# Performance work log

Hardware: AMD Instinct MI355X
Metric: run time of the kernel (lower is better)

## Reference

```python
import jax, jax.numpy as jnp
import numpy as np
from jax import lax

INPUT_SIZE = 256
HIDDEN_SIZE = 512
NUM_LAYERS = 2
T = 2048
B = 64


def setup_inputs() -> dict:
    key = jax.random.key(0)
    k1, k2, k3, k4, k5 = jax.random.split(key, 5)
    fan_g = INPUT_SIZE + HIDDEN_SIZE
    inp = {
        "input": jax.random.normal(k1, (T, B, INPUT_SIZE), dtype=jnp.float32),
        "gate_w": jax.random.uniform(k2, (HIDDEN_SIZE, fan_g), dtype=jnp.float32,
                                     minval=-1.0, maxval=1.0) / np.sqrt(fan_g),
        "gate_b": jax.random.uniform(k3, (HIDDEN_SIZE,), dtype=jnp.float32,
                                     minval=-1.0, maxval=1.0) / np.sqrt(fan_g),
        "out_w": jax.random.uniform(k4, (INPUT_SIZE, HIDDEN_SIZE), dtype=jnp.float32,
                                    minval=-1.0, maxval=1.0) / np.sqrt(HIDDEN_SIZE),
        "out_b": jax.random.uniform(k5, (INPUT_SIZE,), dtype=jnp.float32,
                                    minval=-1.0, maxval=1.0) / np.sqrt(HIDDEN_SIZE),
        "name": 0,  # unused forward arg in the original module
    }
    return inp


def reference(input, gate_w, gate_b, out_w, out_b, name):
    # input: [T, B, input_size]
    batch = input.shape[1]
    h0 = jnp.zeros((batch, HIDDEN_SIZE), dtype=jnp.float32)
    c0 = jnp.zeros((batch, HIDDEN_SIZE), dtype=jnp.float32)

    def step(carry, x_t):
        h, c = carry
        combined = jnp.concatenate([h, x_t], axis=1)          # [B, H+I]
        g = combined @ gate_w.T + gate_b
        s = jax.nn.sigmoid(g)                                 # f = i = o = sigmoid(g)
        ch = jnp.tanh(g)                                      # cell_helper
        c = c * s + ch * s
        h = jnp.tanh(c) * s
        return (h, c), None

    carry = (h0, c0)
    # hidden/cell carry over across layers; every layer re-consumes the same input
    for _ in range(NUM_LAYERS):
        carry, _ = lax.scan(step, carry, input)
    h, _ = carry
    output = h @ out_w.T + out_b                              # [B, input_size]
    return output
```

## Files before the change

### kernel.cpp

```cpp
#include <hip/hip_runtime.h>
#include <stdint.h>

#define T_STEPS 2048
#define BATCH   64
#define IN_SZ   256
#define HID     512
#define FANG    768
#define NLAYER  2
#define TOT_STEPS (T_STEPS*NLAYER)

typedef _Float16 h2 __attribute__((ext_vector_type(2)));
typedef unsigned long long u64;
typedef unsigned int u32;

__device__ __forceinline__ float dot2f(h2 a, h2 b, float c) {
#if __has_builtin(__builtin_amdgcn_fdot2)
    return __builtin_amdgcn_fdot2(a, b, c, false);
#else
    return c + (float)a.x * (float)b.x + (float)a.y * (float)b.y;
#endif
}

__device__ __forceinline__ u32 packh2(float a, float b) {
    h2 t{(_Float16)a, (_Float16)b};
    return __builtin_bit_cast(u32, t);
}
__device__ __forceinline__ h2 bch2(float v) { return __builtin_bit_cast(h2, v); }
__device__ __forceinline__ h2 bch2u(u32 v)  { return __builtin_bit_cast(h2, v); }

__device__ __forceinline__ u64 ld_llc(const u64* p) {
    return __hip_atomic_load(p, __ATOMIC_RELAXED, __HIP_MEMORY_SCOPE_AGENT);
}
__device__ __forceinline__ void st_llc(u64* p, u64 v) {
    __hip_atomic_store(p, v, __ATOMIC_RELAXED, __HIP_MEMORY_SCOPE_AGENT);
}

template<int CTRL>
__device__ __forceinline__ float dpp_add(float x) {
    int xi = __builtin_bit_cast(int, x);
    int yi = __builtin_amdgcn_update_dpp(0, xi, CTRL, 0xf, 0xf, true);
    return x + __builtin_bit_cast(float, yi);
}
__device__ __forceinline__ float reduce4(float x) {
    x = dpp_add<0xB1>(x);
    x = dpp_add<0x4E>(x);
    return x;
}

__global__ __launch_bounds__(256) void xproj_kernel(
    const float* __restrict__ input,
    const float* __restrict__ gate_w,
    const float* __restrict__ gate_b,
    u32* __restrict__ xp16)
{
    __shared__ _Float16 Bs[64][264];
    __shared__ _Float16 As[64][264];

    const int jt = blockIdx.x;
    const int mg = blockIdx.y;
    const int tid = threadIdx.x;
    const int tx = tid & 15, ty = tid >> 4;
    const int j0 = jt * 64;

    #pragma unroll
    for (int l = 0; l < 16; ++l) {
        int e = tid + l * 256;
        int i = e >> 6, kq = e & 63;
        float4 v = *(const float4*)&gate_w[(size_t)(j0 + i) * FANG + HID + kq * 4];
        *(h2*)&Bs[i][kq * 4]     = h2{(_Float16)v.x, (_Float16)v.y};
        *(h2*)&Bs[i][kq * 4 + 2] = h2{(_Float16)v.z, (_Float16)v.w};
    }

    const float4 gb = *(const float4*)&gate_b[j0 + tx * 4];

    for (int mt = 0; mt < 32; ++mt) {
        const int m0 = (mg * 32 + mt) * 64;
        __syncthreads();
        #pragma unroll
        for (int l = 0; l < 16; ++l) {
            int e = tid + l * 256;
            int i = e >> 6, kq = e & 63;
            float4 v = *(const float4*)&input[(size_t)(m0 + i) * IN_SZ + kq * 4];
            *(h2*)&As[i][kq * 4]     = h2{(_Float16)v.x, (_Float16)v.y};
            *(h2*)&As[i][kq * 4 + 2] = h2{(_Float16)v.z, (_Float16)v.w};
        }
        __syncthreads();

        float acc[4][4] = {};
        #pragma unroll
        for (int q = 0; q < 32; ++q) {
            const int k = ((q + tx) & 31) * 8;
            float4 av[4], bv[4];
            #pragma unroll
            for (int i = 0; i < 4; ++i)  av[i] = *(const float4*)&As[ty * 4 + i][k];
            #pragma unroll
            for (int jj = 0; jj < 4; ++jj) bv[jj] = *(const float4*)&Bs[tx * 4 + jj][k];
            #pragma unroll
            for (int i = 0; i < 4; ++i) {
                h2 a0 = bch2(av[i].x), a1 = bch2(av[i].y);
                h2 a2 = bch2(av[i].z), a3 = bch2(av[i].w);
                #pragma unroll
                for (int jj = 0; jj < 4; ++jj) {
                    acc[i][jj] = dot2f(a0, bch2(bv[jj].x), acc[i][jj]);
                    acc[i][jj] = dot2f(a1, bch2(bv[jj].y), acc[i][jj]);
                    acc[i][jj] = dot2f(a2, bch2(bv[jj].z), acc[i][jj]);
                    acc[i][jj] = dot2f(a3, bch2(bv[jj].w), acc[i][jj]);
                }
            }
        }

        #pragma unroll
        for (int i = 0; i < 4; ++i) {
            uint2 ww = { packh2(acc[i][0] + gb.x, acc[i][1] + gb.y),
                         packh2(acc[i][2] + gb.z, acc[i][3] + gb.w) };
            *(uint2*)&xp16[(size_t)(m0 + ty * 4 + i) * 256 + ((j0 + tx * 4) >> 1)] = ww;
        }
    }
}

__global__ __launch_bounds__(512, 2) void lstm_kernel(
    const float* __restrict__ gate_w,
    const u32* __restrict__ xp16,
    u64* __restrict__ hx)
{
    const int blk = blockIdx.x;
    const int s   = blk >> 6;
    const int b   = blk & 63;
    const int tid = threadIdx.x;
    const int r   = tid >> 2;
    const int c   = tid & 3;
    const int j   = s * 128 + r;

    __shared__ u32 hl[2][264];

    h2 w2[64];
    #pragma unroll
    for (int u = 0; u < 16; ++u) {
        const int q = (s * 4 + u) & 15;
        const float* wr = gate_w + (size_t)j * FANG + (q * 16 + c * 4) * 2;
        float4 v0 = *(const float4*)(wr);
        float4 v1 = *(const float4*)(wr + 4);
        w2[u * 4 + 0] = h2{(_Float16)v0.x, (_Float16)v0.y};
        w2[u * 4 + 1] = h2{(_Float16)v0.z, (_Float16)v0.w};
        w2[u * 4 + 2] = h2{(_Float16)v1.x, (_Float16)v1.y};
        w2[u * 4 + 3] = h2{(_Float16)v1.z, (_Float16)v1.w};
    }

    const int si  = tid >> 6;
    const int qs  = si + (si >= s);
    const int prw = qs * 64 + (tid & 63);

    if (tid < 264) hl[0][tid] = 0;

    float cval = 0.0f;

    for (int st = 0; st < TOT_STEPS; ++st) {
        const int t   = st & (T_STEPS - 1);
        const int buf = st & 1;

        u32 xw = 0;
        if (c == 0) xw = xp16[((size_t)t * BATCH + b) * 256 + s * 64 + (r >> 1)];

        const u64* pp = hx + ((size_t)buf * BATCH + b) * 256 + prw;
        u64 pv = 0;
        if (tid < 192) pv = ld_llc(pp);

        __syncthreads();

        float p0 = 0.f, p1 = 0.f, p2 = 0.f, p3 = 0.f;
        #pragma unroll
        for (int u = 0; u < 4; ++u) {
            const int q = s * 4 + u;
            float4 rv = *(const float4*)&hl[buf][q * 16 + c * 4];
            p0 = dot2f(w2[u * 4 + 0], bch2(rv.x), p0);
            p1 = dot2f(w2[u * 4 + 1], bch2(rv.y), p1);
            p2 = dot2f(w2[u * 4 + 2], bch2(rv.z), p2);
            p3 = dot2f(w2[u * 4 + 3], bch2(rv.w), p3);
        }

        if (tid < 192) {
            u64 v = pv;
            int spin = 0;
            while ((u32)(v >> 32) != (u32)st) {
                v = ld_llc(pp);
                if (++spin > (1 << 16)) break;
                if (spin > 64) __builtin_amdgcn_s_sleep(1);
            }
            hl[buf][prw] = (u32)v;
        }
        __syncthreads();

        #pragma unroll
        for (int u = 4; u < 16; ++u) {
            const int q = (s * 4 + u) & 15;
            float4 rv = *(const float4*)&hl[buf][q * 16 + c * 4];
            p0 = dot2f(w2[u * 4 + 0], bch2(rv.x), p0);
            p1 = dot2f(w2[u * 4 + 1], bch2(rv.y), p1);
            p2 = dot2f(w2[u * 4 + 2], bch2(rv.z), p2);
            p3 = dot2f(w2[u * 4 + 3], bch2(rv.w), p3);
        }
        float p = (p0 + p1) + (p2 + p3);
        p = reduce4(p);

        float hf = 0.0f;
        if (c == 0) {
            h2 xp = bch2u(xw);
            float gg = p + (float)((r & 1) ? xp.y : xp.x);
            gg = fminf(fmaxf(gg, -30.0f), 30.0f);
            float sg = 1.0f / (1.0f + __expf(-gg));
            float e2 = __expf(2.0f * gg);
            float ch = (e2 - 1.0f) / (e2 + 1.0f);
            cval = cval * sg + ch * sg;
            float ca = fminf(fmaxf(cval, -15.0f), 15.0f);
            float e3 = __expf(2.0f * ca);
            hf = ((e3 - 1.0f) / (e3 + 1.0f)) * sg;
        }
        float hfo = __shfl_down(hf, 4);
        if ((tid & 7) == 0) {
            const int w = s * 64 + (r >> 1);
            u32 pk = packh2(hf, hfo);
            st_llc(hx + ((size_t)((st + 1) & 1) * BATCH + b) * 256 + w,
                   (u64)pk | ((u64)(u32)(st + 1) << 32));
            hl[buf ^ 1][w] = pk;
        }
    }
}

__global__ __launch_bounds__(256) void out_kernel(
    const u64* __restrict__ hx,
    const float* __restrict__ out_w,
    const float* __restrict__ out_b,
    float* __restrict__ out)
{
    const int b  = blockIdx.x;
    const int jt = threadIdx.x;
    __shared__ float hrow[512];

    {
        u64 v = hx[(size_t)b * 256 + jt];
        h2 pr = bch2u((u32)v);
        hrow[2 * jt]     = (float)pr.x;
        hrow[2 * jt + 1] = (float)pr.y;
    }
    __syncthreads();

    float acc = out_b[jt];
    const float* wr = out_w + (size_t)jt * HID;
    #pragma unroll 8
    for (int k = 0; k < HID; ++k)
        acc += hrow[k] * wr[k];
    out[(size_t)b * IN_SZ + jt] = acc;
}

extern "C" void kernel_launch(void* const* d_in, const int* in_sizes, int n_in,
                              void* d_out, int out_size, void* d_ws, size_t ws_size,
                              hipStream_t stream)
{
    const float* input  = (const float*)d_in[0];
    const float* gate_w = (const float*)d_in[1];
    const float* gate_b = (const float*)d_in[2];
    const float* out_w  = (const float*)d_in[3];
    const float* out_b  = (const float*)d_in[4];
    float* out = (float*)d_out;

    u32* xp16 = (u32*)d_ws;
    const size_t xbytes = (size_t)T_STEPS * BATCH * 256 * sizeof(u32);
    u64* hx = (u64*)((char*)d_ws + xbytes);

    (void)hipMemsetAsync(hx, 0, (size_t)2 * BATCH * 256 * sizeof(u64), stream);

    dim3 g1(8, 64);
    xproj_kernel<<<g1, 256, 0, stream>>>(input, gate_w, gate_b, xp16);
    lstm_kernel<<<256, 512, 0, stream>>>(gate_w, xp16, hx);
    out_kernel<<<64, 256, 0, stream>>>(hx, out_w, out_b, out);
}
```

Before: 5.073 ms.

## Remap LSTM recurrence so each 16-lane group computes four gate rows

Changes the recurrent matvec thread mapping. Before, four lanes shared one gate row and each lane read its own slice of h from LDS. Now each 16-lane group owns four rows, and every float4 of h read from LDS is reused across all four rows, cutting per-step LDS reads by about four times. The cross-lane reduction grows from a 4-lane to a 16-lane rotate-DPP reduction over four accumulators, and the LDS padding is dropped.

```diff
diff --git a/kernel.cpp b/kernel.cpp
--- a/kernel.cpp
+++ b/kernel.cpp
@@ -41,9 +41,11 @@
     int yi = __builtin_amdgcn_update_dpp(0, xi, CTRL, 0xf, 0xf, true);
     return x + __builtin_bit_cast(float, yi);
 }
-__device__ __forceinline__ float reduce4(float x) {
+__device__ __forceinline__ float reduce16(float x) {
     x = dpp_add<0xB1>(x);
     x = dpp_add<0x4E>(x);
+    x = dpp_add<0x124>(x);
+    x = dpp_add<0x128>(x);
     return x;
 }
 
@@ -127,30 +129,33 @@
     const int s   = blk >> 6;
     const int b   = blk & 63;
     const int tid = threadIdx.x;
-    const int r   = tid >> 2;
-    const int c   = tid & 3;
-    const int j   = s * 128 + r;
-
-    __shared__ u32 hl[2][264];
+    const int g   = tid >> 4;
+    const int c   = tid & 15;
+    const int j0  = s * 128 + g * 4;
+
+    __shared__ u32 hl[2][256];
 
     h2 w2[64];
     #pragma unroll
-    for (int u = 0; u < 16; ++u) {
-        const int q = (s * 4 + u) & 15;
-        const float* wr = gate_w + (size_t)j * FANG + (q * 16 + c * 4) * 2;
-        float4 v0 = *(const float4*)(wr);
-        float4 v1 = *(const float4*)(wr + 4);
-        w2[u * 4 + 0] = h2{(_Float16)v0.x, (_Float16)v0.y};
-        w2[u * 4 + 1] = h2{(_Float16)v0.z, (_Float16)v0.w};
-        w2[u * 4 + 2] = h2{(_Float16)v1.x, (_Float16)v1.y};
-        w2[u * 4 + 3] = h2{(_Float16)v1.z, (_Float16)v1.w};
+    for (int u = 0; u < 4; ++u) {
+        const int kb = (((s + u) & 3) * 64 + c * 4) * 2;
+        #pragma unroll
+        for (int rr = 0; rr < 4; ++rr) {
+            const float* wr = gate_w + (size_t)(j0 + rr) * FANG + kb;
+            float4 v0 = *(const float4*)(wr);
+            float4 v1 = *(const float4*)(wr + 4);
+            w2[rr * 16 + u * 4 + 0] = h2{(_Float16)v0.x, (_Float16)v0.y};
+            w2[rr * 16 + u * 4 + 1] = h2{(_Float16)v0.z, (_Float16)v0.w};
+            w2[rr * 16 + u * 4 + 2] = h2{(_Float16)v1.x, (_Float16)v1.y};
+            w2[rr * 16 + u * 4 + 3] = h2{(_Float16)v1.z, (_Float16)v1.w};
+        }
     }
 
     const int si  = tid >> 6;
     const int qs  = si + (si >= s);
     const int prw = qs * 64 + (tid & 63);
 
-    if (tid < 264) hl[0][tid] = 0;
+    if (tid < 256) hl[0][tid] = 0;
 
     float cval = 0.0f;
 
@@ -159,7 +164,7 @@
         const int buf = st & 1;
 
         u32 xw = 0;
-        if (c == 0) xw = xp16[((size_t)t * BATCH + b) * 256 + s * 64 + (r >> 1)];
+        if (c < 4) xw = xp16[((size_t)t * BATCH + b) * 256 + s * 64 + g * 2 + (c >> 1)];
 
         const u64* pp = hx + ((size_t)buf * BATCH + b) * 256 + prw;
         u64 pv = 0;
@@ -167,15 +172,18 @@
 
         __syncthreads();
 
-        float p0 = 0.f, p1 = 0.f, p2 = 0.f, p3 = 0.f;
-        #pragma unroll
-        for (int u = 0; u < 4; ++u) {
-            const int q = s * 4 + u;
-            float4 rv = *(const float4*)&hl[buf][q * 16 + c * 4];
-            p0 = dot2f(w2[u * 4 + 0], bch2(rv.x), p0);
-            p1 = dot2f(w2[u * 4 + 1], bch2(rv.y), p1);
-            p2 = dot2f(w2[u * 4 + 2], bch2(rv.z), p2);
-            p3 = dot2f(w2[u * 4 + 3], bch2(rv.w), p3);
+        float a0 = 0.f, a1 = 0.f, a2 = 0.f, a3 = 0.f;
+        {
+            float4 rv = *(const float4*)&hl[buf][s * 64 + c * 4];
+            h2 x0 = bch2(rv.x), x1 = bch2(rv.y), x2 = bch2(rv.z), x3 = bch2(rv.w);
+            a0 = dot2f(w2[ 0], x0, a0); a0 = dot2f(w2[ 1], x1, a0);
+            a0 = dot2f(w2[ 2], x2, a0); a0 = dot2f(w2[ 3], x3, a0);
+            a1 = dot2f(w2[16], x0, a1); a1 = dot2f(w2[17], x1, a1);
+            a1 = dot2f(w2[18], x2, a1); a1 = dot2f(w2[19], x3, a1);
+            a2 = dot2f(w2[32], x0, a2); a2 = dot2f(w2[33], x1, a2);
+            a2 = dot2f(w2[34], x2, a2); a2 = dot2f(w2[35], x3, a2);
+            a3 = dot2f(w2[48], x0, a3); a3 = dot2f(w2[49], x1, a3);
+            a3 = dot2f(w2[50], x2, a3); a3 = dot2f(w2[51], x3, a3);
         }
 
         if (tid < 192) {
@@ -191,21 +199,29 @@
         __syncthreads();
 
         #pragma unroll
-        for (int u = 4; u < 16; ++u) {
-            const int q = (s * 4 + u) & 15;
-            float4 rv = *(const float4*)&hl[buf][q * 16 + c * 4];
-            p0 = dot2f(w2[u * 4 + 0], bch2(rv.x), p0);
-            p1 = dot2f(w2[u * 4 + 1], bch2(rv.y), p1);
-            p2 = dot2f(w2[u * 4 + 2], bch2(rv.z), p2);
-            p3 = dot2f(w2[u * 4 + 3], bch2(rv.w), p3);
-        }
-        float p = (p0 + p1) + (p2 + p3);
-        p = reduce4(p);
+        for (int u = 1; u < 4; ++u) {
+            float4 rv = *(const float4*)&hl[buf][((s + u) & 3) * 64 + c * 4];
+            h2 x0 = bch2(rv.x), x1 = bch2(rv.y), x2 = bch2(rv.z), x3 = bch2(rv.w);
+            a0 = dot2f(w2[     u*4+0], x0, a0); a0 = dot2f(w2[     u*4+1], x1, a0);
+            a0 = dot2f(w2[     u*4+2], x2, a0); a0 = dot2f(w2[     u*4+3], x3, a0);
+            a1 = dot2f(w2[16 + u*4+0], x0, a1); a1 = dot2f(w2[16 + u*4+1], x1, a1);
+            a1 = dot2f(w2[16 + u*4+2], x2, a1); a1 = dot2f(w2[16 + u*4+3], x3, a1);
+            a2 = dot2f(w2[32 + u*4+0], x0, a2); a2 = dot2f(w2[32 + u*4+1], x1, a2);
+            a2 = dot2f(w2[32 + u*4+2], x2, a2); a2 = dot2f(w2[32 + u*4+3], x3, a2);
+            a3 = dot2f(w2[48 + u*4+0], x0, a3); a3 = dot2f(w2[48 + u*4+1], x1, a3);
+            a3 = dot2f(w2[48 + u*4+2], x2, a3); a3 = dot2f(w2[48 + u*4+3], x3, a3);
+        }
+
+        a0 = reduce16(a0);
+        a1 = reduce16(a1);
+        a2 = reduce16(a2);
+        a3 = reduce16(a3);
 
         float hf = 0.0f;
-        if (c == 0) {
+        if (c < 4) {
+            float p = (c == 0) ? a0 : (c == 1) ? a1 : (c == 2) ? a2 : a3;
             h2 xp = bch2u(xw);
-            float gg = p + (float)((r & 1) ? xp.y : xp.x);
+            float gg = p + (float)((c & 1) ? xp.y : xp.x);
             gg = fminf(fmaxf(gg, -30.0f), 30.0f);
             float sg = 1.0f / (1.0f + __expf(-gg));
             float e2 = __expf(2.0f * gg);
@@ -215,9 +231,9 @@
             float e3 = __expf(2.0f * ca);
             hf = ((e3 - 1.0f) / (e3 + 1.0f)) * sg;
         }
-        float hfo = __shfl_down(hf, 4);
-        if ((tid & 7) == 0) {
-            const int w = s * 64 + (r >> 1);
+        float hfo = __shfl_down(hf, 1);
+        if (c == 0 || c == 2) {
+            const int w = s * 64 + g * 2 + (c >> 1);
             u32 pk = packh2(hf, hfo);
             st_llc(hx + ((size_t)((st + 1) & 1) * BATCH + b) * 256 + w,
                    (u64)pk | ((u64)(u32)(st + 1) << 32));
```

New measurement: 4.936 ms. 2.7% less time.
